# Optimization experiments

Measured on AMD Instinct MI355X. Metric: run time of the kernel, lower is better.

The kernel has to match this reference:

```python
import jax, jax.numpy as jnp
import numpy as np

EPS = 1e-5

def layer_norm(x, w, b):
    mu = jnp.mean(x, axis=-1, keepdims=True)
    var = jnp.mean(jnp.square(x - mu), axis=-1, keepdims=True)
    return (x - mu) * jax.lax.rsqrt(var + EPS) * w + b

def setup_inputs() -> dict:
    key = jax.random.key(0)
    ks = jax.random.split(key, 16)
    B, N, c_z, c_h = 1, 512, 128, 128
    s_z = 1.0 / np.sqrt(c_z)
    s_h = 1.0 / np.sqrt(c_h)
    return {
        "z": jax.random.normal(ks[0], (B, N, N, c_z), jnp.float32),
        "mask": jnp.ones((B, N, N), jnp.float32),
        "norm_in_w": jnp.ones((c_z,), jnp.float32),
        "norm_in_b": jnp.zeros((c_z,), jnp.float32),
        "a_p_w": jax.random.normal(ks[1], (c_h, c_z), jnp.float32) * s_z,
        "a_p_b": jnp.zeros((c_h,), jnp.float32),
        "a_g_w": jax.random.normal(ks[2], (c_h, c_z), jnp.float32) * s_z,
        "a_g_b": jnp.ones((c_h,), jnp.float32),
        "b_p_w": jax.random.normal(ks[3], (c_h, c_z), jnp.float32) * s_z,
        "b_p_b": jnp.zeros((c_h,), jnp.float32),
        "b_g_w": jax.random.normal(ks[4], (c_h, c_z), jnp.float32) * s_z,
        "b_g_b": jnp.ones((c_h,), jnp.float32),
        "g_w": jax.random.normal(ks[5], (c_z, c_z), jnp.float32) * s_z,
        "g_b": jnp.ones((c_z,), jnp.float32),
        "z_w": jax.random.normal(ks[6], (c_z, c_h), jnp.float32) * s_h,
        "z_b": jnp.zeros((c_z,), jnp.float32),
        "norm_out_w": jnp.ones((c_h,), jnp.float32),
        "norm_out_b": jnp.zeros((c_h,), jnp.float32),
    }

OUTGOING = True

def reference(z, mask, norm_in_w, norm_in_b, a_p_w, a_p_b, a_g_w, a_g_b,
              b_p_w, b_p_b, b_g_w, b_g_b, g_w, g_b, z_w, z_b,
              norm_out_w, norm_out_b):
    # z: [B, N, N, c_z]; mask: [B, N, N]
    m = mask[..., None]  # [B, N, N, 1]
    zn = layer_norm(z, norm_in_w, norm_in_b)
    # gated projections (nn.Linear layout: W is [out, in])
    a = m * jax.nn.sigmoid(zn @ a_g_w.T + a_g_b) * (zn @ a_p_w.T + a_p_b)
    b = m * jax.nn.sigmoid(zn @ b_g_w.T + b_g_b) * (zn @ b_p_w.T + b_p_b)
    if OUTGOING:
        # x[i,j,c] = sum_k a[i,k,c] * b[j,k,c]
        x = jnp.einsum('bikc,bjkc->bijc', a, b)
    else:
        x = jnp.einsum('bkic,bkjc->bijc', a, b)
    x = layer_norm(x, norm_out_w, norm_out_b)
    x = x @ z_w.T + z_b
    g = jax.nn.sigmoid(zn @ g_w.T + g_b)
    return x * g
```

## Files before the change

### kernel.cpp

```cpp
#include <hip/hip_runtime.h>
#include <stddef.h>

#define NN 512
#define CC 128
#define NPOS (NN*NN)
#define CPITCH (NPOS + 512)

typedef unsigned short u16;
typedef unsigned int   u32;
typedef u16  u16x4  __attribute__((ext_vector_type(4)));
typedef u16  u16x8  __attribute__((ext_vector_type(8)));
typedef __bf16 bf16x8 __attribute__((ext_vector_type(8)));
typedef float f32x4  __attribute__((ext_vector_type(4)));

__device__ __forceinline__ float b2f(u16 u) {
    union { u32 i; float f; } w; w.i = ((u32)u) << 16; return w.f;
}
__device__ __forceinline__ u16 f2b(float f) {
    return __builtin_bit_cast(u16, (__bf16)f);
}
__device__ __forceinline__ float sigm(float x) { return 1.0f / (1.0f + __expf(-x)); }

__device__ __forceinline__ void gld16(const u16* g, u16* l) {
    __builtin_amdgcn_global_load_lds(
        (const __attribute__((address_space(1))) u32*)g,
        (__attribute__((address_space(3))) u32*)l, 16, 0, 0);
}

struct W6 { const float* p[6]; };

__global__ __launch_bounds__(256) void k0_pack(W6 w, u16* __restrict__ dst)
{
    const int i = blockIdx.x * 256 + threadIdx.x;
    const int mt = i >> 14, r = i & 16383;
    const int cb = r >> 11, ks = (r >> 9) & 3, lane = (r >> 3) & 63, j = r & 7;
    const int row = cb * 16 + (lane & 15);
    const int col = ks * 32 + (lane >> 4) * 8 + j;
    dst[i] = f2b(w.p[mt][row * 128 + col]);
}

__global__ __launch_bounds__(128) void k1_ln_proj(
    const float* __restrict__ z,  const float* __restrict__ mask,
    const float* __restrict__ wi, const float* __restrict__ bi,
    const u16* __restrict__ wpk,
    const float* __restrict__ agb, const float* __restrict__ apb,
    const float* __restrict__ bgb, const float* __restrict__ bpb,
    u16* __restrict__ a_cm, u16* __restrict__ b_cm,
    u16* __restrict__ zn_pm)
{
    __shared__ u16 zn[64][136];
    const int tid = threadIdx.x;
    const size_t p0 = (size_t)blockIdx.x * 64;

    {
        const float* zt = z + p0 * CC;
        const int g  = tid >> 5;
        const int c4 = (tid & 31) * 4;
        const f32x4 wi4 = *(const f32x4*)(wi + c4);
        const f32x4 bi4 = *(const f32x4*)(bi + c4);
        f32x4 v[16];
        #pragma unroll
        for (int h = 0; h < 16; ++h)
            v[h] = *(const f32x4*)(zt + h * 512 + tid * 4);
        #pragma unroll
        for (int h = 0; h < 16; ++h) {
            float s  = (v[h][0] + v[h][1]) + (v[h][2] + v[h][3]);
            float s2 = (v[h][0]*v[h][0] + v[h][1]*v[h][1])
                     + (v[h][2]*v[h][2] + v[h][3]*v[h][3]);
            #pragma unroll
            for (int ms = 1; ms <= 16; ms <<= 1) {
                s  += __shfl_xor(s,  ms);
                s2 += __shfl_xor(s2, ms);
            }
            const float mu   = s * (1.0f / CC);
            const float rstd = rsqrtf(s2 * (1.0f / CC) - mu * mu + 1e-5f);
            u16x4 o4;
            #pragma unroll
            for (int e = 0; e < 4; ++e) {
                const float nw = rstd * wi4[e];
                o4[e] = f2b(v[h][e] * nw + __builtin_fmaf(-mu, nw, bi4[e]));
            }
            *(u16x4*)&zn[h * 4 + g][c4] = o4;
            if (zn_pm)
                *(u16x4*)(zn_pm + (p0 + h * 4 + g) * CC + c4) = o4;
        }
    }
    __syncthreads();

    const int wave = tid >> 6, lane = tid & 63;
    const int m = lane & 15, q = lane >> 4;

    bf16x8 af[2][4];
    #pragma unroll
    for (int t = 0; t < 2; ++t)
        #pragma unroll
        for (int ks = 0; ks < 4; ++ks)
            af[t][ks] = *(const bf16x8*)&zn[wave * 32 + t * 16 + m][ks * 32 + q * 8];

    f32x4 mkv[2];
    #pragma unroll
    for (int t = 0; t < 2; ++t)
        mkv[t] = *(const f32x4*)(mask + p0 + wave * 32 + t * 16 + q * 4);

    const float* Bv[4] = { agb, apb, bgb, bpb };

    for (int cb = 0; cb < 8; ++cb) {
        const int o = cb * 16 + m;
        f32x4 res[4][2];
        #pragma unroll
        for (int mt = 0; mt < 4; ++mt) {
            const float bvv = Bv[mt][o];
            #pragma unroll
            for (int t = 0; t < 2; ++t) res[mt][t] = f32x4{ bvv, bvv, bvv, bvv };
            const u16* wp = wpk + ((size_t)((mt * 8 + cb) * 4)) * 512 + (size_t)lane * 8;
            bf16x8 wf[4];
            #pragma unroll
            for (int ks = 0; ks < 4; ++ks) wf[ks] = *(const bf16x8*)(wp + ks * 512);
            #pragma unroll
            for (int ks = 0; ks < 4; ++ks)
                #pragma unroll
                for (int t = 0; t < 2; ++t)
                    res[mt][t] = __builtin_amdgcn_mfma_f32_16x16x32_bf16(
                                   af[t][ks], wf[ks], res[mt][t], 0, 0, 0);
        }
        #pragma unroll
        for (int t = 0; t < 2; ++t) {
            u16x4 av, bv;
            #pragma unroll
            for (int r = 0; r < 4; ++r) {
                const float mk = mkv[t][r];
                av[r] = f2b(mk * sigm(res[0][t][r]) * res[1][t][r]);
                bv[r] = f2b(mk * sigm(res[2][t][r]) * res[3][t][r]);
            }
            const size_t off = (size_t)o * CPITCH + p0 + wave * 32 + t * 16 + q * 4;
            *(u16x4*)(a_cm + off) = av;
            *(u16x4*)(b_cm + off) = bv;
        }
    }
}

__global__ __launch_bounds__(256) void k2_gemm(
    const u16* __restrict__ A, const u16* __restrict__ B, u16* __restrict__ X)
{
    __shared__ u16 As[2][128][32];
    __shared__ u16 Bs[2][128][32];
    const int tid = threadIdx.x;
    const int bx  = blockIdx.x;
    const int xcd  = bx & 7;
    const int slot = bx >> 3;
    const int c    = (slot >> 4) * 8 + xcd;
    const int tile = slot & 15;
    const int i0   = (tile >> 2) * 128;
    const int j0   = (tile & 3) * 128;
    const size_t cbase = (size_t)c * CPITCH;
    const u16* Ac = A + cbase;
    const u16* Bc = B + cbase;

    const int wave = tid >> 6, lane = tid & 63;
    const int wm = wave >> 1, wn = wave & 1;
    const int m = lane & 15, q = lane >> 4;

    f32x4 acc[4][4];
    const f32x4 zero = { 0.f, 0.f, 0.f, 0.f };
    #pragma unroll
    for (int mt = 0; mt < 4; ++mt)
        #pragma unroll
        for (int nt = 0; nt < 4; ++nt) acc[mt][nt] = zero;

    for (int kt = 0; kt < 8; ++kt) {
        __syncthreads();
        #pragma unroll
        for (int ps = 0; ps < 4; ++ps) {
            const int id   = ps * 256 + tid;
            const int half = id >> 9;
            const int rw   = (id >> 2) & 127;
            const int g    = (id & 3) ^ ((rw >> 1) & 3);
            const size_t goff = (size_t)(kt * 64 + half * 32 + g * 8);
            gld16(Ac + (size_t)(i0 + rw) * NN + goff, &As[0][0][0] + id * 8);
            gld16(Bc + (size_t)(j0 + rw) * NN + goff, &Bs[0][0][0] + id * 8);
        }
        __syncthreads();
        #pragma unroll
        for (int ks = 0; ks < 2; ++ks) {
            bf16x8 af[4], bf[4];
            #pragma unroll
            for (int mt = 0; mt < 4; ++mt) {
                const int row = wm * 64 + mt * 16 + m;
                const int slt = q ^ ((row >> 1) & 3);
                af[mt] = *(const bf16x8*)&As[ks][row][slt * 8];
            }
            #pragma unroll
            for (int nt = 0; nt < 4; ++nt) {
                const int row = wn * 64 + nt * 16 + m;
                const int slt = q ^ ((row >> 1) & 3);
                bf[nt] = *(const bf16x8*)&Bs[ks][row][slt * 8];
            }
            #pragma unroll
            for (int mt = 0; mt < 4; ++mt)
                #pragma unroll
                for (int nt = 0; nt < 4; ++nt)
                    acc[mt][nt] = __builtin_amdgcn_mfma_f32_16x16x32_bf16(
                                    af[mt], bf[nt], acc[mt][nt], 0, 0, 0);
        }
    }

    #pragma unroll
    for (int mt = 0; mt < 4; ++mt) {
        #pragma unroll
        for (int r = 0; r < 4; ++r) {
            const int i = i0 + wm * 64 + mt * 16 + q * 4 + r;
            #pragma unroll
            for (int nt = 0; nt < 4; ++nt) {
                const int j = j0 + wn * 64 + nt * 16 + m;
                X[cbase + (size_t)i * NN + j] = f2b(acc[mt][nt][r]);
            }
        }
    }
}

__global__ __launch_bounds__(256) void k3_out_zn(
    float* __restrict__ out, const u16* __restrict__ x_cm,
    const u16* __restrict__ zn_pm,
    const float* __restrict__ wo, const float* __restrict__ bo,
    const u16* __restrict__ wpk,
    const float* __restrict__ gbv, const float* __restrict__ zbv)
{
    __shared__ u16 A[128][136];
    __shared__ u16 Bt[128][136];
    const int tid = threadIdx.x;
    const size_t p0 = (size_t)blockIdx.x * 128;
    const int wave = tid >> 6, lane = tid & 63;
    const int m = lane & 15, q = lane >> 4;
    const int pl = tid >> 1, ht = tid & 1;

    {
        const int c = tid >> 1, seg = tid & 1;
        #pragma unroll
        for (int e = 0; e < 8; ++e) {
            u16x8 vv = *(const u16x8*)(x_cm + (size_t)c * CPITCH + p0 + seg * 64 + e * 8);
            *(u16x8*)&Bt[c][seg * 64 + e * 8] = vv;
        }
    }
    bf16x8 afz[2][4];
    #pragma unroll
    for (int t = 0; t < 2; ++t)
        #pragma unroll
        for (int ks = 0; ks < 4; ++ks)
            afz[t][ks] = *(const bf16x8*)(zn_pm
                           + (p0 + wave * 32 + t * 16 + m) * CC + ks * 32 + q * 8);
    __syncthreads();

    {
        float v[64];
        #pragma unroll
        for (int e = 0; e < 64; ++e) v[e] = b2f(Bt[ht * 64 + e][pl]);
        float s = 0.f, s2 = 0.f;
        #pragma unroll
        for (int e = 0; e < 64; ++e) { s += v[e]; s2 += v[e] * v[e]; }
        s  += __shfl_xor(s, 1);
        s2 += __shfl_xor(s2, 1);
        const float mu   = s * (1.0f / CC);
        const float rstd = rsqrtf(s2 * (1.0f / CC) - mu * mu + 1e-5f);
        #pragma unroll
        for (int h = 0; h < 8; ++h) {
            u16x8 o8;
            #pragma unroll
            for (int e = 0; e < 8; ++e) {
                const int c = ht * 64 + h * 8 + e;
                o8[e] = f2b((v[h * 8 + e] - mu) * rstd * wo[c] + bo[c]);
            }
            *(u16x8*)&A[pl][ht * 64 + h * 8] = o8;
        }
    }
    __syncthreads();

    bf16x8 afx[2][4];
    #pragma unroll
    for (int t = 0; t < 2; ++t)
        #pragma unroll
        for (int ks = 0; ks < 4; ++ks)
            afx[t][ks] = *(const bf16x8*)&A[wave * 32 + t * 16 + m][ks * 32 + q * 8];

    for (int cb = 0; cb < 8; ++cb) {
        const int o = cb * 16 + m;
        const float gb0 = gbv[o], zb0 = zbv[o];
        f32x4 accg[2], accx[2];
        #pragma unroll
        for (int t = 0; t < 2; ++t) {
            accg[t] = f32x4{ gb0, gb0, gb0, gb0 };
            accx[t] = f32x4{ zb0, zb0, zb0, zb0 };
        }
        const u16* wpg = wpk + ((size_t)((4 * 8 + cb) * 4)) * 512 + (size_t)lane * 8;
        const u16* wpz = wpk + ((size_t)((5 * 8 + cb) * 4)) * 512 + (size_t)lane * 8;
        bf16x8 wg[4], wz[4];
        #pragma unroll
        for (int ks = 0; ks < 4; ++ks) {
            wg[ks] = *(const bf16x8*)(wpg + ks * 512);
            wz[ks] = *(const bf16x8*)(wpz + ks * 512);
        }
        #pragma unroll
        for (int ks = 0; ks < 4; ++ks)
            #pragma unroll
            for (int t = 0; t < 2; ++t) {
                accg[t] = __builtin_amdgcn_mfma_f32_16x16x32_bf16(
                            afz[t][ks], wg[ks], accg[t], 0, 0, 0);
                accx[t] = __builtin_amdgcn_mfma_f32_16x16x32_bf16(
                            afx[t][ks], wz[ks], accx[t], 0, 0, 0);
            }
        #pragma unroll
        for (int t = 0; t < 2; ++t)
            #pragma unroll
            for (int r = 0; r < 4; ++r) {
                const size_t p = p0 + wave * 32 + t * 16 + q * 4 + r;
                out[p * CC + o] = accx[t][r] * sigm(accg[t][r]);
            }
    }
}

__global__ __launch_bounds__(256) void k3_out(
    float* __restrict__ out, const u16* __restrict__ x_cm,
    const float* __restrict__ z,
    const float* __restrict__ wi, const float* __restrict__ bi,
    const float* __restrict__ wo, const float* __restrict__ bo,
    const u16* __restrict__ wpk,
    const float* __restrict__ gbv, const float* __restrict__ zbv)
{
    __shared__ u16 A[128][136];
    __shared__ u16 Bt[128][136];
    const int tid = threadIdx.x;
    const size_t p0 = (size_t)blockIdx.x * 128;
    const int wave = tid >> 6, lane = tid & 63;
    const int m = lane & 15, q = lane >> 4;
    const int pl = tid >> 1, ht = tid & 1;

    {
        const float* zr = z + (p0 + pl) * CC + ht * 64;
        float v[64];
        #pragma unroll
        for (int h = 0; h < 16; ++h) {
            f32x4 t = *(const f32x4*)(zr + h * 4);
            #pragma unroll
            for (int e = 0; e < 4; ++e) v[h * 4 + e] = t[e];
        }
        float s = 0.f, s2 = 0.f;
        #pragma unroll
        for (int e = 0; e < 64; ++e) { s += v[e]; s2 += v[e] * v[e]; }
        s  += __shfl_xor(s, 1);
        s2 += __shfl_xor(s2, 1);
        const float mu   = s * (1.0f / CC);
        const float rstd = rsqrtf(s2 * (1.0f / CC) - mu * mu + 1e-5f);
        #pragma unroll
        for (int h = 0; h < 8; ++h) {
            u16x8 o8;
            #pragma unroll
            for (int e = 0; e < 8; ++e) {
                const int c = ht * 64 + h * 8 + e;
                o8[e] = f2b((v[h * 8 + e] - mu) * rstd * wi[c] + bi[c]);
            }
            *(u16x8*)&A[pl][ht * 64 + h * 8] = o8;
        }
    }
    {
        const int c = tid >> 1, seg = tid & 1;
        #pragma unroll
        for (int e = 0; e < 8; ++e) {
            u16x8 vv = *(const u16x8*)(x_cm + (size_t)c * CPITCH + p0 + seg * 64 + e * 8);
            *(u16x8*)&Bt[c][seg * 64 + e * 8] = vv;
        }
    }
    __syncthreads();

    bf16x8 afz[2][4];
    #pragma unroll
    for (int t = 0; t < 2; ++t)
        #pragma unroll
        for (int ks = 0; ks < 4; ++ks)
            afz[t][ks] = *(const bf16x8*)&A[wave * 32 + t * 16 + m][ks * 32 + q * 8];
    __syncthreads();

    {
        float v[64];
        #pragma unroll
        for (int e = 0; e < 64; ++e) v[e] = b2f(Bt[ht * 64 + e][pl]);
        float s = 0.f, s2 = 0.f;
        #pragma unroll
        for (int e = 0; e < 64; ++e) { s += v[e]; s2 += v[e] * v[e]; }
        s  += __shfl_xor(s, 1);
        s2 += __shfl_xor(s2, 1);
        const float mu   = s * (1.0f / CC);
        const float rstd = rsqrtf(s2 * (1.0f / CC) - mu * mu + 1e-5f);
        #pragma unroll
        for (int h = 0; h < 8; ++h) {
            u16x8 o8;
            #pragma unroll
            for (int e = 0; e < 8; ++e) {
                const int c = ht * 64 + h * 8 + e;
                o8[e] = f2b((v[h * 8 + e] - mu) * rstd * wo[c] + bo[c]);
            }
            *(u16x8*)&A[pl][ht * 64 + h * 8] = o8;
        }
    }
    __syncthreads();

    bf16x8 afx[2][4];
    #pragma unroll
    for (int t = 0; t < 2; ++t)
        #pragma unroll
        for (int ks = 0; ks < 4; ++ks)
            afx[t][ks] = *(const bf16x8*)&A[wave * 32 + t * 16 + m][ks * 32 + q * 8];

    for (int cb = 0; cb < 8; ++cb) {
        const int o = cb * 16 + m;
        const float gb0 = gbv[o], zb0 = zbv[o];
        f32x4 accg[2], accx[2];
        #pragma unroll
        for (int t = 0; t < 2; ++t) {
            accg[t] = f32x4{ gb0, gb0, gb0, gb0 };
            accx[t] = f32x4{ zb0, zb0, zb0, zb0 };
        }
        const u16* wpg = wpk + ((size_t)((4 * 8 + cb) * 4)) * 512 + (size_t)lane * 8;
        const u16* wpz = wpk + ((size_t)((5 * 8 + cb) * 4)) * 512 + (size_t)lane * 8;
        bf16x8 wg[4], wz[4];
        #pragma unroll
        for (int ks = 0; ks < 4; ++ks) {
            wg[ks] = *(const bf16x8*)(wpg + ks * 512);
            wz[ks] = *(const bf16x8*)(wpz + ks * 512);
        }
        #pragma unroll
        for (int ks = 0; ks < 4; ++ks)
            #pragma unroll
            for (int t = 0; t < 2; ++t) {
                accg[t] = __builtin_amdgcn_mfma_f32_16x16x32_bf16(
                            afz[t][ks], wg[ks], accg[t], 0, 0, 0);
                accx[t] = __builtin_amdgcn_mfma_f32_16x16x32_bf16(
                            afx[t][ks], wz[ks], accx[t], 0, 0, 0);
            }
        #pragma unroll
        for (int t = 0; t < 2; ++t)
            #pragma unroll
            for (int r = 0; r < 4; ++r) {
                const size_t p = p0 + wave * 32 + t * 16 + q * 4 + r;
                out[p * CC + o] = accx[t][r] * sigm(accg[t][r]);
            }
    }
}

extern "C" void kernel_launch(void* const* d_in, const int* in_sizes, int n_in,
                              void* d_out, int out_size, void* d_ws, size_t ws_size,
                              hipStream_t stream)
{
    const float* z    = (const float*)d_in[0];
    const float* mask = (const float*)d_in[1];
    const float* wi   = (const float*)d_in[2];
    const float* bi   = (const float*)d_in[3];
    const float* apw  = (const float*)d_in[4];
    const float* apb  = (const float*)d_in[5];
    const float* agw  = (const float*)d_in[6];
    const float* agb  = (const float*)d_in[7];
    const float* bpw  = (const float*)d_in[8];
    const float* bpb  = (const float*)d_in[9];
    const float* bgw  = (const float*)d_in[10];
    const float* bgb  = (const float*)d_in[11];
    const float* gw   = (const float*)d_in[12];
    const float* gb   = (const float*)d_in[13];
    const float* zw   = (const float*)d_in[14];
    const float* zb   = (const float*)d_in[15];
    const float* wo   = (const float*)d_in[16];
    const float* bo   = (const float*)d_in[17];

    u16* a_cm = (u16*)d_ws;
    u16* b_cm = a_cm + (size_t)CC * CPITCH;
    u16* x_cm = b_cm + (size_t)CC * CPITCH;
    u16* w_pk = x_cm + (size_t)CC * CPITCH;
    u16* zn_pm = w_pk + (size_t)6 * 16384;
    float* out = (float*)d_out;

    const size_t need_zn =
        ((size_t)CC * CPITCH * 3 + 6 * 16384 + (size_t)NPOS * CC) * sizeof(u16);
    const bool use_zn = (ws_size == 0) || (ws_size >= need_zn);
    if (!use_zn) zn_pm = nullptr;

    W6 w6; w6.p[0] = agw; w6.p[1] = apw; w6.p[2] = bgw; w6.p[3] = bpw;
    w6.p[4] = gw; w6.p[5] = zw;

    k0_pack<<<6 * 16384 / 256, 256, 0, stream>>>(w6, w_pk);
    k1_ln_proj<<<NPOS / 64, 128, 0, stream>>>(z, mask, wi, bi, w_pk,
                                              agb, apb, bgb, bpb, a_cm, b_cm, zn_pm);
    k2_gemm<<<128 * 16, 256, 0, stream>>>(a_cm, b_cm, x_cm);
    if (use_zn)
        k3_out_zn<<<NPOS / 128, 256, 0, stream>>>(out, x_cm, zn_pm, wo, bo,
                                                  w_pk, gb, zb);
    else
        k3_out<<<NPOS / 128, 256, 0, stream>>>(out, x_cm, z, wi, bi, wo, bo,
                                               w_pk, gb, zb);
}
```

Baseline: 480.5 us.

## Restructure projection kernel so weights stay in registers across larger position tiles

```diff
diff --git a/kernel.cpp b/kernel.cpp
--- a/kernel.cpp
+++ b/kernel.cpp
@@ -5,6 +5,7 @@
 #define CC 128
 #define NPOS (NN*NN)
 #define CPITCH (NPOS + 512)
+#define POSB 256
 
 typedef unsigned short u16;
 typedef unsigned int   u32;
@@ -39,7 +40,7 @@
     dst[i] = f2b(w.p[mt][row * 128 + col]);
 }
 
-__global__ __launch_bounds__(128) void k1_ln_proj(
+__global__ __launch_bounds__(256) void k1_ln_proj(
     const float* __restrict__ z,  const float* __restrict__ mask,
     const float* __restrict__ wi, const float* __restrict__ bi,
     const u16* __restrict__ wpk,
@@ -48,25 +49,24 @@
     u16* __restrict__ a_cm, u16* __restrict__ b_cm,
     u16* __restrict__ zn_pm)
 {
-    __shared__ u16 zn[64][136];
+    __shared__ u16   zn[POSB][136];
+    __shared__ float mk_lds[POSB];
     const int tid = threadIdx.x;
-    const size_t p0 = (size_t)blockIdx.x * 64;
+    const size_t p0 = (size_t)blockIdx.x * POSB;
+
+    mk_lds[tid] = mask[p0 + tid];
 
     {
-        const float* zt = z + p0 * CC;
         const int g  = tid >> 5;
         const int c4 = (tid & 31) * 4;
         const f32x4 wi4 = *(const f32x4*)(wi + c4);
         const f32x4 bi4 = *(const f32x4*)(bi + c4);
-        f32x4 v[16];
-        #pragma unroll
-        for (int h = 0; h < 16; ++h)
-            v[h] = *(const f32x4*)(zt + h * 512 + tid * 4);
-        #pragma unroll
-        for (int h = 0; h < 16; ++h) {
-            float s  = (v[h][0] + v[h][1]) + (v[h][2] + v[h][3]);
-            float s2 = (v[h][0]*v[h][0] + v[h][1]*v[h][1])
-                     + (v[h][2]*v[h][2] + v[h][3]*v[h][3]);
+        #pragma unroll 4
+        for (int h = 0; h < 32; ++h) {
+            const int row = h * 8 + g;
+            const f32x4 v = *(const f32x4*)(z + (p0 + row) * CC + c4);
+            float s  = (v[0] + v[1]) + (v[2] + v[3]);
+            float s2 = (v[0]*v[0] + v[1]*v[1]) + (v[2]*v[2] + v[3]*v[3]);
             #pragma unroll
             for (int ms = 1; ms <= 16; ms <<= 1) {
                 s  += __shfl_xor(s,  ms);
@@ -78,61 +78,67 @@
             #pragma unroll
             for (int e = 0; e < 4; ++e) {
                 const float nw = rstd * wi4[e];
-                o4[e] = f2b(v[h][e] * nw + __builtin_fmaf(-mu, nw, bi4[e]));
-            }
-            *(u16x4*)&zn[h * 4 + g][c4] = o4;
+                o4[e] = f2b(v[e] * nw + __builtin_fmaf(-mu, nw, bi4[e]));
+            }
+            *(u16x4*)&zn[row][c4] = o4;
             if (zn_pm)
-                *(u16x4*)(zn_pm + (p0 + h * 4 + g) * CC + c4) = o4;
-        }
-    }
-    __syncthreads();
+                *(u16x4*)(zn_pm + (p0 + row) * CC + c4) = o4;
+        }
+    }
 
     const int wave = tid >> 6, lane = tid & 63;
     const int m = lane & 15, q = lane >> 4;
 
-    bf16x8 af[2][4];
-    #pragma unroll
-    for (int t = 0; t < 2; ++t)
-        #pragma unroll
-        for (int ks = 0; ks < 4; ++ks)
-            af[t][ks] = *(const bf16x8*)&zn[wave * 32 + t * 16 + m][ks * 32 + q * 8];
-
-    f32x4 mkv[2];
-    #pragma unroll
-    for (int t = 0; t < 2; ++t)
-        mkv[t] = *(const f32x4*)(mask + p0 + wave * 32 + t * 16 + q * 4);
-
-    const float* Bv[4] = { agb, apb, bgb, bpb };
-
-    for (int cb = 0; cb < 8; ++cb) {
-        const int o = cb * 16 + m;
-        f32x4 res[4][2];
+    bf16x8 wreg[2][4][4];
+    float  bias[2][4];
+    #pragma unroll
+    for (int c2 = 0; c2 < 2; ++c2) {
+        const int cb = wave * 2 + c2;
+        const int o  = cb * 16 + m;
+        bias[c2][0] = agb[o]; bias[c2][1] = apb[o];
+        bias[c2][2] = bgb[o]; bias[c2][3] = bpb[o];
         #pragma unroll
         for (int mt = 0; mt < 4; ++mt) {
-            const float bvv = Bv[mt][o];
-            #pragma unroll
-            for (int t = 0; t < 2; ++t) res[mt][t] = f32x4{ bvv, bvv, bvv, bvv };
-            const u16* wp = wpk + ((size_t)((mt * 8 + cb) * 4)) * 512 + (size_t)lane * 8;
-            bf16x8 wf[4];
-            #pragma unroll
-            for (int ks = 0; ks < 4; ++ks) wf[ks] = *(const bf16x8*)(wp + ks * 512);
+            const u16* wp = wpk + ((size_t)((mt * 8 + cb) * 4)) * 512
+                                + (size_t)lane * 8;
+            #pragma unroll
+            for (int ks = 0; ks < 4; ++ks)
+                wreg[c2][mt][ks] = *(const bf16x8*)(wp + ks * 512);
+        }
+    }
+    __syncthreads();
+
+    for (int t = 0; t < POSB / 16; ++t) {
+        const int pos0 = t * 16;
+        bf16x8 af[4];
+        #pragma unroll
+        for (int ks = 0; ks < 4; ++ks)
+            af[ks] = *(const bf16x8*)&zn[pos0 + m][ks * 32 + q * 8];
+        const f32x4 mk4 = *(const f32x4*)&mk_lds[pos0 + q * 4];
+
+        #pragma unroll
+        for (int c2 = 0; c2 < 2; ++c2) {
+            f32x4 res[4];
+            #pragma unroll
+            for (int mt = 0; mt < 4; ++mt) {
+                const float bv = bias[c2][mt];
+                res[mt] = f32x4{ bv, bv, bv, bv };
+            }
             #pragma unroll
             for (int ks = 0; ks < 4; ++ks)
                 #pragma unroll
-                for (int t = 0; t < 2; ++t)
-                    res[mt][t] = __builtin_amdgcn_mfma_f32_16x16x32_bf16(
-                                   af[t][ks], wf[ks], res[mt][t], 0, 0, 0);
-        }
-        #pragma unroll
-        for (int t = 0; t < 2; ++t) {
+                for (int mt = 0; mt < 4; ++mt)
+                    res[mt] = __builtin_amdgcn_mfma_f32_16x16x32_bf16(
+                                af[ks], wreg[c2][mt][ks], res[mt], 0, 0, 0);
             u16x4 av, bv;
             #pragma unroll
             for (int r = 0; r < 4; ++r) {
-                const float mk = mkv[t][r];
-                av[r] = f2b(mk * sigm(res[0][t][r]) * res[1][t][r]);
-                bv[r] = f2b(mk * sigm(res[2][t][r]) * res[3][t][r]);
-            }
-            const size_t off = (size_t)o * CPITCH + p0 + wave * 32 + t * 16 + q * 4;
+                const float mk = mk4[r];
+                av[r] = f2b(mk * sigm(res[0][r]) * res[1][r]);
+                bv[r] = f2b(mk * sigm(res[2][r]) * res[3][r]);
+            }
+            const int o = (wave * 2 + c2) * 16 + m;
+            const size_t off = (size_t)o * CPITCH + p0 + pos0 + q * 4;
             *(u16x4*)(a_cm + off) = av;
             *(u16x4*)(b_cm + off) = bv;
         }
@@ -484,8 +490,8 @@
     w6.p[4] = gw; w6.p[5] = zw;
 
     k0_pack<<<6 * 16384 / 256, 256, 0, stream>>>(w6, w_pk);
-    k1_ln_proj<<<NPOS / 64, 128, 0, stream>>>(z, mask, wi, bi, w_pk,
-                                              agb, apb, bgb, bpb, a_cm, b_cm, zn_pm);
+    k1_ln_proj<<<NPOS / POSB, 256, 0, stream>>>(z, mask, wi, bi, w_pk,
+                                                agb, apb, bgb, bpb, a_cm, b_cm, zn_pm);
     k2_gemm<<<128 * 16, 256, 0, stream>>>(a_cm, b_cm, x_cm);
     if (use_zn)
         k3_out_zn<<<NPOS / 128, 256, 0, stream>>>(out, x_cm, zn_pm, wo, bo,
```

After: 484.3 us. Within noise of the previous version (+0.8%).

## Fold output LayerNorm affine and normalization into output projection epilogue

Applied to the files above, without the earlier changes.

```diff
diff --git a/kernel.cpp b/kernel.cpp
--- a/kernel.cpp
+++ b/kernel.cpp
@@ -29,14 +29,32 @@
 
 struct W6 { const float* p[6]; };
 
-__global__ __launch_bounds__(256) void k0_pack(W6 w, u16* __restrict__ dst)
+__global__ __launch_bounds__(256) void k0_pack(W6 w, const float* __restrict__ wo,
+                                               u16* __restrict__ dst)
 {
     const int i = blockIdx.x * 256 + threadIdx.x;
     const int mt = i >> 14, r = i & 16383;
     const int cb = r >> 11, ks = (r >> 9) & 3, lane = (r >> 3) & 63, j = r & 7;
     const int row = cb * 16 + (lane & 15);
     const int col = ks * 32 + (lane >> 4) * 8 + j;
-    dst[i] = f2b(w.p[mt][row * 128 + col]);
+    float v = w.p[mt][row * 128 + col];
+    if (wo && mt == 5) v *= wo[col];
+    dst[i] = f2b(v);
+}
+
+__global__ __launch_bounds__(128) void k0_s12(
+    const float* __restrict__ zw, const float* __restrict__ wo,
+    const float* __restrict__ bo, float* __restrict__ s12)
+{
+    const int o = threadIdx.x;
+    float s1 = 0.f, s2 = 0.f;
+    #pragma unroll 4
+    for (int c = 0; c < 128; ++c) {
+        const float zv = zw[o * 128 + c];
+        s1 += bo[c] * zv;
+        s2 += wo[c] * zv;
+    }
+    s12[o] = s1; s12[128 + o] = s2;
 }
 
 __global__ __launch_bounds__(128) void k1_ln_proj(
@@ -218,27 +236,27 @@
     }
 }
 
-__global__ __launch_bounds__(256) void k3_out_zn(
+__global__ __launch_bounds__(256) void k3_out_fold(
     float* __restrict__ out, const u16* __restrict__ x_cm,
     const u16* __restrict__ zn_pm,
-    const float* __restrict__ wo, const float* __restrict__ bo,
-    const u16* __restrict__ wpk,
+    const u16* __restrict__ wpk, const float* __restrict__ s12,
     const float* __restrict__ gbv, const float* __restrict__ zbv)
 {
-    __shared__ u16 A[128][136];
-    __shared__ u16 Bt[128][136];
+    __shared__ u16   XT[128][136];
+    __shared__ float mu_l[128], rs_l[128];
     const int tid = threadIdx.x;
     const size_t p0 = (size_t)blockIdx.x * 128;
     const int wave = tid >> 6, lane = tid & 63;
     const int m = lane & 15, q = lane >> 4;
-    const int pl = tid >> 1, ht = tid & 1;
 
     {
         const int c = tid >> 1, seg = tid & 1;
         #pragma unroll
         for (int e = 0; e < 8; ++e) {
             u16x8 vv = *(const u16x8*)(x_cm + (size_t)c * CPITCH + p0 + seg * 64 + e * 8);
-            *(u16x8*)&Bt[c][seg * 64 + e * 8] = vv;
+            #pragma unroll
+            for (int j = 0; j < 8; ++j)
+                XT[seg * 64 + e * 8 + j][c] = vv[j];
         }
     }
     bf16x8 afz[2][4];
@@ -248,47 +266,61 @@
         for (int ks = 0; ks < 4; ++ks)
             afz[t][ks] = *(const bf16x8*)(zn_pm
                            + (p0 + wave * 32 + t * 16 + m) * CC + ks * 32 + q * 8);
-    __syncthreads();
-
-    {
-        float v[64];
-        #pragma unroll
-        for (int e = 0; e < 64; ++e) v[e] = b2f(Bt[ht * 64 + e][pl]);
-        float s = 0.f, s2 = 0.f;
-        #pragma unroll
-        for (int e = 0; e < 64; ++e) { s += v[e]; s2 += v[e] * v[e]; }
-        s  += __shfl_xor(s, 1);
-        s2 += __shfl_xor(s2, 1);
-        const float mu   = s * (1.0f / CC);
-        const float rstd = rsqrtf(s2 * (1.0f / CC) - mu * mu + 1e-5f);
-        #pragma unroll
-        for (int h = 0; h < 8; ++h) {
-            u16x8 o8;
-            #pragma unroll
-            for (int e = 0; e < 8; ++e) {
-                const int c = ht * 64 + h * 8 + e;
-                o8[e] = f2b((v[h * 8 + e] - mu) * rstd * wo[c] + bo[c]);
-            }
-            *(u16x8*)&A[pl][ht * 64 + h * 8] = o8;
-        }
-    }
-    __syncthreads();
-
-    bf16x8 afx[2][4];
-    #pragma unroll
-    for (int t = 0; t < 2; ++t)
-        #pragma unroll
-        for (int ks = 0; ks < 4; ++ks)
-            afx[t][ks] = *(const bf16x8*)&A[wave * 32 + t * 16 + m][ks * 32 + q * 8];
-
+    float s1z[8], s2r[8], gb8[8];
+    #pragma unroll
     for (int cb = 0; cb < 8; ++cb) {
         const int o = cb * 16 + m;
-        const float gb0 = gbv[o], zb0 = zbv[o];
+        s1z[cb] = s12[o] + zbv[o];
+        s2r[cb] = s12[128 + o];
+        gb8[cb] = gbv[o];
+    }
+    __syncthreads();
+
+    {
+        const int g = tid >> 5, l32 = tid & 31;
+        #pragma unroll 4
+        for (int it = 0; it < 16; ++it) {
+            const int row = it * 8 + g;
+            const u16x4 xv = *(const u16x4*)&XT[row][l32 * 4];
+            const float x0 = b2f(xv[0]), x1 = b2f(xv[1]),
+                        x2 = b2f(xv[2]), x3 = b2f(xv[3]);
+            float s  = (x0 + x1) + (x2 + x3);
+            float s2 = (x0*x0 + x1*x1) + (x2*x2 + x3*x3);
+            #pragma unroll
+            for (int ms = 1; ms <= 16; ms <<= 1) {
+                s  += __shfl_xor(s,  ms);
+                s2 += __shfl_xor(s2, ms);
+            }
+            const float mu   = s * (1.0f / CC);
+            const float rstd = rsqrtf(s2 * (1.0f / CC) - mu * mu + 1e-5f);
+            if (l32 == 0) { mu_l[row] = mu; rs_l[row] = rstd; }
+        }
+    }
+    __syncthreads();
+
+    bf16x8 afx[2][4];
+    #pragma unroll
+    for (int t = 0; t < 2; ++t)
+        #pragma unroll
+        for (int ks = 0; ks < 4; ++ks)
+            afx[t][ks] = *(const bf16x8*)&XT[wave * 32 + t * 16 + m][ks * 32 + q * 8];
+
+    f32x4 mu4[2], rs4[2];
+    #pragma unroll
+    for (int t = 0; t < 2; ++t) {
+        mu4[t] = *(const f32x4*)&mu_l[wave * 32 + t * 16 + q * 4];
+        rs4[t] = *(const f32x4*)&rs_l[wave * 32 + t * 16 + q * 4];
+    }
+
+    for (int cb = 0; cb < 8; ++cb) {
+        const int o = cb * 16 + m;
         f32x4 accg[2], accx[2];
+        const f32x4 zero = { 0.f, 0.f, 0.f, 0.f };
         #pragma unroll
         for (int t = 0; t < 2; ++t) {
-            accg[t] = f32x4{ gb0, gb0, gb0, gb0 };
-            accx[t] = f32x4{ zb0, zb0, zb0, zb0 };
+            const float g0 = gb8[cb];
+            accg[t] = f32x4{ g0, g0, g0, g0 };
+            accx[t] = zero;
         }
         const u16* wpg = wpk + ((size_t)((4 * 8 + cb) * 4)) * 512 + (size_t)lane * 8;
         const u16* wpz = wpk + ((size_t)((5 * 8 + cb) * 4)) * 512 + (size_t)lane * 8;
@@ -312,7 +344,9 @@
             #pragma unroll
             for (int r = 0; r < 4; ++r) {
                 const size_t p = p0 + wave * 32 + t * 16 + q * 4 + r;
-                out[p * CC + o] = accx[t][r] * sigm(accg[t][r]);
+                const float y = rs4[t][r] * (accx[t][r] - mu4[t][r] * s2r[cb])
+                              + s1z[cb];
+                out[p * CC + o] = y * sigm(accg[t][r]);
             }
     }
 }
@@ -473,23 +507,27 @@
     u16* x_cm = b_cm + (size_t)CC * CPITCH;
     u16* w_pk = x_cm + (size_t)CC * CPITCH;
     u16* zn_pm = w_pk + (size_t)6 * 16384;
+    float* s12 = (float*)(zn_pm + (size_t)NPOS * CC);
     float* out = (float*)d_out;
 
     const size_t need_zn =
-        ((size_t)CC * CPITCH * 3 + 6 * 16384 + (size_t)NPOS * CC) * sizeof(u16);
+        ((size_t)CC * CPITCH * 3 + 6 * 16384 + (size_t)NPOS * CC) * sizeof(u16)
+        + 256 * sizeof(float);
     const bool use_zn = (ws_size == 0) || (ws_size >= need_zn);
     if (!use_zn) zn_pm = nullptr;
 
     W6 w6; w6.p[0] = agw; w6.p[1] = apw; w6.p[2] = bgw; w6.p[3] = bpw;
     w6.p[4] = gw; w6.p[5] = zw;
 
-    k0_pack<<<6 * 16384 / 256, 256, 0, stream>>>(w6, w_pk);
+    k0_pack<<<6 * 16384 / 256, 256, 0, stream>>>(w6, use_zn ? wo : nullptr, w_pk);
+    if (use_zn)
+        k0_s12<<<1, 128, 0, stream>>>(zw, wo, bo, s12);
     k1_ln_proj<<<NPOS / 64, 128, 0, stream>>>(z, mask, wi, bi, w_pk,
                                               agb, apb, bgb, bpb, a_cm, b_cm, zn_pm);
     k2_gemm<<<128 * 16, 256, 0, stream>>>(a_cm, b_cm, x_cm);
     if (use_zn)
-        k3_out_zn<<<NPOS / 128, 256, 0, stream>>>(out, x_cm, zn_pm, wo, bo,
-                                                  w_pk, gb, zb);
+        k3_out_fold<<<NPOS / 128, 256, 0, stream>>>(out, x_cm, zn_pm,
+                                                    w_pk, s12, gb, zb);
     else
         k3_out<<<NPOS / 128, 256, 0, stream>>>(out, x_cm, z, wi, bi, wo, bo,
                                                w_pk, gb, zb);
```

After: 495.5 us. 1.03x slower.
